# Kernel optimization log

Hardware: AMD Instinct MI355X
Metric: run time of the kernel (lower is better)

Reference implementation:

```python
import jax, jax.numpy as jnp
import numpy as np

B, N, D = 8, 4096, 256


def setup_inputs() -> dict:
    key = jax.random.key(0)
    ks = jax.random.split(key, 4)
    seq = jax.random.normal(ks[0], (B, N, D), dtype=jnp.float32)
    W_fts = jax.random.normal(ks[1], (D, D), dtype=jnp.float32) * (1.0 / np.sqrt(D))
    w_f1 = jax.random.normal(ks[2], (D, 1), dtype=jnp.float32) * (1.0 / np.sqrt(D))
    b_f1 = jnp.zeros((1,), dtype=jnp.float32)
    w_f2 = jax.random.normal(ks[3], (D, 1), dtype=jnp.float32) * (1.0 / np.sqrt(D))
    b_f2 = jnp.zeros((1,), dtype=jnp.float32)
    bias = jnp.zeros((1,), dtype=jnp.float32)
    return {"seq": seq, "W_fts": W_fts, "w_f1": w_f1, "b_f1": b_f1,
            "w_f2": w_f2, "b_f2": b_f2, "bias": bias}


def reference(seq, W_fts, w_f1, b_f1, w_f2, b_f2, bias):
    # seq: [B, N, D]
    seq_fts = jnp.einsum('bnd,de->bne', seq, W_fts)          # values, [B, N, D]
    f_1 = seq @ w_f1 + b_f1                                   # [B, N, 1]
    f_2 = seq @ w_f2 + b_f2                                   # [B, N, 1]
    logits = f_1 + jnp.swapaxes(f_2, 1, 2)                    # broadcast add -> [B, N, N]
    coefs = jax.nn.softmax(jax.nn.leaky_relu(logits, negative_slope=0.01), axis=-1)
    vals = jnp.einsum('bnm,bmd->bnd', coefs, seq_fts)         # [B, N, D]
    ret = vals + bias
    return jax.nn.relu(ret)
```

## Files before the change

kernel.cpp:

```cpp
#include <hip/hip_runtime.h>
#include <hip/hip_bf16.h>
#include <math.h>

#define B 8
#define N 4096
#define D 256
#define BN (B*N)
#define NSUP 64
#define NS1 65
#define NR1 4097

typedef __attribute__((ext_vector_type(8))) short bf16x8;
typedef __attribute__((ext_vector_type(4))) float f32x4;

#define GLD16(src, dst) __builtin_amdgcn_global_load_lds( \
    (const __attribute__((address_space(1))) void*)(src), \
    (__attribute__((address_space(3))) void*)(dst), 16, 0, 0)

__device__ __forceinline__ ushort bf16_hi(float x) {
  __hip_bfloat16 h = __float2bfloat16(x);
  return *(ushort*)&h;
}
__device__ __forceinline__ ushort bf16_lo(float x) {
  __hip_bfloat16 h = __float2bfloat16(x);
  float hf = __bfloat162float(h);
  __hip_bfloat16 l = __float2bfloat16(x - hf);
  return *(ushort*)&l;
}

__global__ __launch_bounds__(256) void k_f1f2w(const float* __restrict__ seq,
    const float* __restrict__ w1, const float* __restrict__ b1,
    const float* __restrict__ w2, const float* __restrict__ b2,
    const float* __restrict__ W, float* __restrict__ f1, float* __restrict__ f2,
    int* __restrict__ rank, ushort* __restrict__ W3) {
  if (blockIdx.x >= BN/4) {
    int n = blockIdx.x - BN/4;
    int k = threadIdx.x;
    float x = W[(size_t)k * D + n];
    ushort hu = bf16_hi(x), lu = bf16_lo(x);
    W3[(size_t)n * 768 + k] = hu;
    W3[(size_t)n * 768 + 256 + k] = lu;
    W3[(size_t)n * 768 + 512 + k] = hu;
    return;
  }
  int wave = threadIdx.x >> 6;
  int lane = threadIdx.x & 63;
  long row = (long)blockIdx.x * 4 + wave;
  float4 v = ((const float4*)(seq + row * D))[lane];
  float4 a = ((const float4*)w1)[lane];
  float4 b = ((const float4*)w2)[lane];
  float s1 = v.x*a.x + v.y*a.y + v.z*a.z + v.w*a.w;
  float s2 = v.x*b.x + v.y*b.y + v.z*b.z + v.w*b.w;
  for (int off = 32; off; off >>= 1) {
    s1 += __shfl_xor(s1, off, 64);
    s2 += __shfl_xor(s2, off, 64);
  }
  if (lane == 0) {
    f1[row] = s1 + b1[0];
    f2[row] = s2 + b2[0];
    rank[row] = 0;
  }
}

__global__ __launch_bounds__(256) void k_rank_count(const float* __restrict__ f2,
    int* __restrict__ rank) {
  __shared__ unsigned long long skey[256];
  int b = blockIdx.z;
  int tid = threadIdx.x;
  const float* fb = f2 + (long)b * N;
  int p = blockIdx.y * 256 + tid;
  unsigned int up = __float_as_uint(fb[p]);
  up ^= (unsigned int)(((int)up >> 31) | 0x80000000);
  skey[tid] = ((unsigned long long)up << 12) | (unsigned)p;
  unsigned long long kj[4];
  int jbase = blockIdx.x * 1024;
  #pragma unroll
  for (int q = 0; q < 4; ++q) {
    int j = jbase + q * 256 + tid;
    unsigned int uj = __float_as_uint(fb[j]);
    uj ^= (unsigned int)(((int)uj >> 31) | 0x80000000);
    kj[q] = ((unsigned long long)uj << 12) | (unsigned)j;
  }
  __syncthreads();
  int c[4] = {0, 0, 0, 0};
  const ulonglong2* sk2 = (const ulonglong2*)skey;
  #pragma unroll 4
  for (int pp = 0; pp < 128; ++pp) {
    ulonglong2 kk = sk2[pp];
    #pragma unroll
    for (int q = 0; q < 4; ++q) {
      c[q] += (kk.x < kj[q]) ? 1 : 0;
      c[q] += (kk.y < kj[q]) ? 1 : 0;
    }
  }
  #pragma unroll
  for (int q = 0; q < 4; ++q)
    atomicAdd(&rank[(long)b * N + jbase + q * 256 + tid], c[q]);
}

__global__ __launch_bounds__(256) void k_scatter(const float* __restrict__ f2,
    const int* __restrict__ rank, float* __restrict__ sF2, int* __restrict__ sIdx,
    float* __restrict__ e2lo, float* __restrict__ e2hi) {
  long idx = (long)blockIdx.x * 256 + threadIdx.x;
  int b = (int)(idx >> 12);
  int j = (int)(idx & (N - 1));
  float v = f2[idx];
  int cnt = rank[idx];
  long o = (long)b * N + cnt;
  sF2[o] = v;
  sIdx[o] = j;
  e2lo[o] = expf(0.01f * v);
  e2hi[o] = expf(v);
}

__global__ __launch_bounds__(256) void k_mfma(const float* __restrict__ seq,
    const int* __restrict__ sIdx, const ushort* __restrict__ W3,
    const float* __restrict__ e2lo, const float* __restrict__ e2hi,
    float* __restrict__ RelLo, float* __restrict__ RelHi,
    float* __restrict__ ZrelLo, float* __restrict__ ZrelHi,
    float* __restrict__ SupBaseLo, float* __restrict__ SupBaseHi,
    float* __restrict__ SupZlo, float* __restrict__ SupZhi) {
  __shared__ __align__(16) char smem[64 * 256 * 4];
  ushort (*As)[72] = (ushort(*)[72])smem;
  ushort (*Bs)[64] = (ushort(*)[64])(smem + 64 * 72 * 2);
  int tid = threadIdx.x;
  int wid = tid >> 6, lane = tid & 63;
  int mBase = blockIdx.x * 64;
  int b = mBase >> 12;
  int ar = tid >> 2, aq = tid & 3;
  const float* aSrc = seq + (((size_t)(b << 12)) + sIdx[mBase + ar]) * D + aq * 16;
  int lr = lane >> 3;
  int lcSw = (((lane & 7) ^ (lr & 7))) * 8;
  int wr = wid >> 1, wc = wid & 1, g = lane >> 4, r16 = lane & 15;
  int bswz = r16 & 7;

  f32x4 acc[2][8];
  #pragma unroll
  for (int m = 0; m < 2; ++m)
    #pragma unroll
    for (int n = 0; n < 8; ++n) {
      acc[m][n][0] = 0.f; acc[m][n][1] = 0.f; acc[m][n][2] = 0.f; acc[m][n][3] = 0.f;
    }

  for (int kt = 0; kt < 768; kt += 64) {
    int acol = kt & 255;
    float4 xv[4];
    #pragma unroll
    for (int i = 0; i < 4; ++i) xv[i] = *(const float4*)(aSrc + acol + i * 4);
    ushort ou[16];
    if (kt < 512) {
      #pragma unroll
      for (int i = 0; i < 4; ++i) {
        ou[i*4+0] = bf16_hi(xv[i].x); ou[i*4+1] = bf16_hi(xv[i].y);
        ou[i*4+2] = bf16_hi(xv[i].z); ou[i*4+3] = bf16_hi(xv[i].w);
      }
    } else {
      #pragma unroll
      for (int i = 0; i < 4; ++i) {
        ou[i*4+0] = bf16_lo(xv[i].x); ou[i*4+1] = bf16_lo(xv[i].y);
        ou[i*4+2] = bf16_lo(xv[i].z); ou[i*4+3] = bf16_lo(xv[i].w);
      }
    }
    __syncthreads();
    #pragma unroll
    for (int i = 0; i < 4; ++i)
      *(ushort4*)&As[ar][aq * 16 + i * 4] =
          make_ushort4(ou[i*4+0], ou[i*4+1], ou[i*4+2], ou[i*4+3]);
    #pragma unroll
    for (int q = 0; q < 8; ++q) {
      int r0 = q * 32 + wid * 8;
      GLD16(W3 + (size_t)(r0 + lr) * 768 + kt + lcSw, &Bs[r0][0]);
    }
    __syncthreads();
    #pragma unroll
    for (int kk = 0; kk < 64; kk += 32) {
      bf16x8 av[2], bv[8];
      #pragma unroll
      for (int m = 0; m < 2; ++m)
        av[m] = *(const bf16x8*)&As[wr*32 + m*16 + r16][kk + g*8];
      int jb = (kk >> 3) + g;
      int jj = jb ^ bswz;
      #pragma unroll
      for (int n = 0; n < 8; ++n) {
        int row = wc*128 + n*16 + r16;
        bv[n] = *(const bf16x8*)((const char*)Bs + row * 128 + jj * 16);
      }
      #pragma unroll
      for (int m = 0; m < 2; ++m)
        #pragma unroll
        for (int n = 0; n < 8; ++n)
          acc[m][n] = __builtin_amdgcn_mfma_f32_16x16x32_bf16(av[m], bv[n], acc[m][n], 0, 0, 0);
    }
  }

  __syncthreads();
  float (*Vt)[256] = (float(*)[256])smem;
  int cswz = (g & 3) << 2;
  #pragma unroll
  for (int m = 0; m < 2; ++m)
    #pragma unroll
    for (int n = 0; n < 8; ++n) {
      int col = (wc*128 + n*16 + r16) ^ cswz;
      #pragma unroll
      for (int j = 0; j < 4; ++j)
        Vt[wr*32 + m*16 + g*4 + j][col] = acc[m][n][j];
    }
  __syncthreads();
  int d = tid;
  int s = (mBase >> 6) & 63;
  size_t rb = (size_t)mBase;
  float rl = 0.f, rh = 0.f;
  float* pLo = RelLo + ((size_t)b * NR1 + (size_t)s * 64) * D + d;
  float* pHi = RelHi + ((size_t)b * NR1 + (size_t)s * 64) * D + d;
  #pragma unroll 8
  for (int r = 0; r < 64; ++r) {
    float wlo = e2lo[rb + r], whi = e2hi[rb + r];
    float v = Vt[r][d ^ (((r >> 2) & 3) << 2)];
    pLo[(size_t)r * D] = rl;
    pHi[(size_t)r * D] = rh;
    rl += wlo * v; rh += whi * v;
  }
  SupBaseLo[((size_t)b * NS1 + s) * D + d] = rl;
  SupBaseHi[((size_t)b * NS1 + s) * D + d] = rh;
  if (tid == 0) {
    float z = 0.f;
    #pragma unroll 8
    for (int r = 0; r < 64; ++r) { ZrelLo[(size_t)b * NR1 + s*64 + r] = z; z += e2lo[rb + r]; }
    SupZlo[b*NS1+s] = z;
  } else if (tid == 64) {
    float z = 0.f;
    #pragma unroll 8
    for (int r = 0; r < 64; ++r) { ZrelHi[(size_t)b * NR1 + s*64 + r] = z; z += e2hi[rb + r]; }
    SupZhi[b*NS1+s] = z;
  }
}

__global__ __launch_bounds__(256) void k_supscan(float* __restrict__ SupBaseLo,
    float* __restrict__ SupBaseHi, float* __restrict__ SupZlo,
    float* __restrict__ SupZhi, float* __restrict__ RelLo, float* __restrict__ RelHi,
    float* __restrict__ ZrelLo, float* __restrict__ ZrelHi) {
  int b = blockIdx.x, t = threadIdx.x;
  if (t < 64) {
    float4* lo = (float4*)SupBaseLo + (size_t)b * NS1 * 64 + t;
    float4* hi = (float4*)SupBaseHi + (size_t)b * NS1 * 64 + t;
    float4 rl = {0,0,0,0}, rh = {0,0,0,0};
    for (int s = 0; s < NSUP; s += 8) {
      float4 tl[8], th[8];
      #pragma unroll
      for (int u = 0; u < 8; ++u) { tl[u] = lo[(size_t)(s+u)*64]; th[u] = hi[(size_t)(s+u)*64]; }
      #pragma unroll
      for (int u = 0; u < 8; ++u) {
        lo[(size_t)(s+u)*64] = rl; hi[(size_t)(s+u)*64] = rh;
        rl.x+=tl[u].x; rl.y+=tl[u].y; rl.z+=tl[u].z; rl.w+=tl[u].w;
        rh.x+=th[u].x; rh.y+=th[u].y; rh.z+=th[u].z; rh.w+=th[u].w;
      }
    }
    lo[(size_t)NSUP*64] = rl;
    hi[(size_t)NSUP*64] = rh;
  } else if (t < 128) {
    float4 z = {0,0,0,0};
    ((float4*)RelLo)[((size_t)b * NR1 + 4096) * 64 + (t - 64)] = z;
  } else if (t < 192) {
    float4 z = {0,0,0,0};
    ((float4*)RelHi)[((size_t)b * NR1 + 4096) * 64 + (t - 128)] = z;
  } else if (t == 192) {
    float r = 0.f;
    for (int s = 0; s < NSUP; ++s) { float x = SupZlo[b*NS1+s]; SupZlo[b*NS1+s] = r; r += x; }
    SupZlo[b*NS1+NSUP] = r;
    ZrelLo[(size_t)b * NR1 + 4096] = 0.f;
  } else if (t == 193) {
    float r = 0.f;
    for (int s = 0; s < NSUP; ++s) { float x = SupZhi[b*NS1+s]; SupZhi[b*NS1+s] = r; r += x; }
    SupZhi[b*NS1+NSUP] = r;
    ZrelHi[(size_t)b * NR1 + 4096] = 0.f;
  }
}

__global__ __launch_bounds__(256) void k_combine2(const float* __restrict__ f1,
    const float* __restrict__ sF2,
    const float* __restrict__ RelLo, const float* __restrict__ RelHi,
    const float* __restrict__ SupBaseLo, const float* __restrict__ SupBaseHi,
    const float* __restrict__ SupZlo, const float* __restrict__ SupZhi,
    const float* __restrict__ ZrelLo, const float* __restrict__ ZrelHi,
    const float* __restrict__ bias, float* __restrict__ out) {
  int wid = threadIdx.x >> 6, lane = threadIdx.x & 63;
  size_t i = (size_t)blockIdx.x * 4 + wid;
  int b = (int)(i >> 12);
  float f1v = f1[i];
  const float* sb = sF2 + ((size_t)b << 12);
  float t = -f1v;
  int lo = 0, hi = N;
  while (lo < hi) { int mid = (lo + hi) >> 1; if (sb[mid] <= t) lo = mid + 1; else hi = mid; }
  int k = lo;
  int s = k >> 6;
  float a = expf(f1v), cc = expf(0.01f * f1v);
  float4 rl4  = ((const float4*)RelLo)[((size_t)b * NR1 + k) * 64 + lane];
  float4 rh4  = ((const float4*)RelHi)[((size_t)b * NR1 + k) * 64 + lane];
  float4 sblo = ((const float4*)SupBaseLo)[((size_t)b * NS1 + s) * 64 + lane];
  float4 sbhi = ((const float4*)SupBaseHi)[((size_t)b * NS1 + s) * 64 + lane];
  float4 pht  = ((const float4*)SupBaseHi)[((size_t)b * NS1 + NSUP) * 64 + lane];
  float Zlo = SupZlo[b*NS1+s] + ZrelLo[(size_t)b * NR1 + k];
  float Zhi = SupZhi[b*NS1+NSUP] - SupZhi[b*NS1+s] - ZrelHi[(size_t)b * NR1 + k];
  float Z = a * Zhi + cc * Zlo;
  float rz = 1.f / Z;
  float bs = bias[0];
  float4 o4;
  o4.x = fmaxf((a*(pht.x - sbhi.x - rh4.x) + cc*(sblo.x + rl4.x)) * rz + bs, 0.f);
  o4.y = fmaxf((a*(pht.y - sbhi.y - rh4.y) + cc*(sblo.y + rl4.y)) * rz + bs, 0.f);
  o4.z = fmaxf((a*(pht.z - sbhi.z - rh4.z) + cc*(sblo.z + rl4.z)) * rz + bs, 0.f);
  o4.w = fmaxf((a*(pht.w - sbhi.w - rh4.w) + cc*(sblo.w + rl4.w)) * rz + bs, 0.f);
  ((float4*)out)[i * 64 + lane] = o4;
}

extern "C" void kernel_launch(void* const* d_in, const int* in_sizes, int n_in,
                              void* d_out, int out_size, void* d_ws, size_t ws_size,
                              hipStream_t stream) {
  const float* seq  = (const float*)d_in[0];
  const float* Wf   = (const float*)d_in[1];
  const float* w1   = (const float*)d_in[2];
  const float* b1   = (const float*)d_in[3];
  const float* w2   = (const float*)d_in[4];
  const float* b2   = (const float*)d_in[5];
  const float* bias = (const float*)d_in[6];
  float* out = (float*)d_out;

  size_t need = (size_t)4 * (7*BN + 2*(size_t)B*NR1*D + 2*(size_t)B*NS1*D
              + 2*B*NS1 + 2*(size_t)B*NR1) + (size_t)256*768*2;
  if (ws_size < need) return;

  float* f1   = (float*)d_ws;
  float* f2   = f1 + BN;
  float* sF2  = f2 + BN;
  float* e2lo = sF2 + BN;
  float* e2hi = e2lo + BN;
  int* sIdx   = (int*)(e2hi + BN);
  int* rank   = sIdx + BN;
  float* RelLo = (float*)(rank + BN);
  float* RelHi = RelLo + (size_t)B * NR1 * D;
  float* SupBaseLo = RelHi + (size_t)B * NR1 * D;
  float* SupBaseHi = SupBaseLo + (size_t)B * NS1 * D;
  float* SupZlo = SupBaseHi + (size_t)B * NS1 * D;
  float* SupZhi = SupZlo + B * NS1;
  float* ZrelLo = SupZhi + B * NS1;
  float* ZrelHi = ZrelLo + (size_t)B * NR1;
  ushort* W3 = (ushort*)(ZrelHi + (size_t)B * NR1);

  k_f1f2w<<<dim3(BN/4 + 256), 256, 0, stream>>>(seq, w1, b1, w2, b2, Wf,
      f1, f2, rank, W3);
  k_rank_count<<<dim3(N/1024, N/256, B), 256, 0, stream>>>(f2, rank);
  k_scatter<<<dim3(BN/256), 256, 0, stream>>>(f2, rank, sF2, sIdx, e2lo, e2hi);
  k_mfma<<<dim3(BN/64), 256, 0, stream>>>(seq, sIdx, W3, e2lo, e2hi,
      RelLo, RelHi, ZrelLo, ZrelHi, SupBaseLo, SupBaseHi, SupZlo, SupZhi);
  k_supscan<<<dim3(B), 256, 0, stream>>>(SupBaseLo, SupBaseHi, SupZlo, SupZhi,
      RelLo, RelHi, ZrelLo, ZrelHi);
  k_combine2<<<dim3(BN/4), 256, 0, stream>>>(f1, sF2,
      RelLo, RelHi, SupBaseLo, SupBaseHi, SupZlo, SupZhi, ZrelLo, ZrelHi, bias, out);
}
```

Measured before the change: 91.53 us.

## Fuse scatter and superblock scan into producers via last-block atomics; interleave Rel

```diff
diff --git a/kernel.cpp b/kernel.cpp
--- a/kernel.cpp
+++ b/kernel.cpp
@@ -32,7 +32,7 @@
     const float* __restrict__ w1, const float* __restrict__ b1,
     const float* __restrict__ w2, const float* __restrict__ b2,
     const float* __restrict__ W, float* __restrict__ f1, float* __restrict__ f2,
-    int* __restrict__ rank, ushort* __restrict__ W3) {
+    int* __restrict__ rank, int* __restrict__ done, ushort* __restrict__ W3) {
   if (blockIdx.x >= BN/4) {
     int n = blockIdx.x - BN/4;
     int k = threadIdx.x;
@@ -43,6 +43,7 @@
     W3[(size_t)n * 768 + 512 + k] = hu;
     return;
   }
+  if (blockIdx.x == 0 && threadIdx.x < 64) done[threadIdx.x] = 0;
   int wave = threadIdx.x >> 6;
   int lane = threadIdx.x & 63;
   long row = (long)blockIdx.x * 4 + wave;
@@ -63,8 +64,10 @@
 }
 
 __global__ __launch_bounds__(256) void k_rank_count(const float* __restrict__ f2,
-    int* __restrict__ rank) {
+    int* __restrict__ rank, int* __restrict__ doneRank, float* __restrict__ sF2,
+    int* __restrict__ sIdx, float* __restrict__ e2lo, float* __restrict__ e2hi) {
   __shared__ unsigned long long skey[256];
+  __shared__ int lastFlag;
   int b = blockIdx.z;
   int tid = threadIdx.x;
   const float* fb = f2 + (long)b * N;
@@ -96,31 +99,37 @@
   #pragma unroll
   for (int q = 0; q < 4; ++q)
     atomicAdd(&rank[(long)b * N + jbase + q * 256 + tid], c[q]);
-}
-
-__global__ __launch_bounds__(256) void k_scatter(const float* __restrict__ f2,
-    const int* __restrict__ rank, float* __restrict__ sF2, int* __restrict__ sIdx,
-    float* __restrict__ e2lo, float* __restrict__ e2hi) {
-  long idx = (long)blockIdx.x * 256 + threadIdx.x;
-  int b = (int)(idx >> 12);
-  int j = (int)(idx & (N - 1));
-  float v = f2[idx];
-  int cnt = rank[idx];
-  long o = (long)b * N + cnt;
-  sF2[o] = v;
-  sIdx[o] = j;
-  e2lo[o] = expf(0.01f * v);
-  e2hi[o] = expf(v);
+  __threadfence();
+  if (tid == 0) {
+    int old = atomicAdd(&doneRank[b * 4 + blockIdx.x], 1);
+    lastFlag = (old == 15);
+  }
+  __syncthreads();
+  if (lastFlag) {
+    #pragma unroll
+    for (int q = 0; q < 4; ++q) {
+      int j = jbase + q * 256 + tid;
+      long idx = (long)b * N + j;
+      int cnt = atomicAdd(&rank[idx], 0);
+      float v = fb[j];
+      long o = (long)b * N + cnt;
+      sF2[o] = v;
+      sIdx[o] = j;
+      e2lo[o] = expf(0.01f * v);
+      e2hi[o] = expf(v);
+    }
+  }
 }
 
 __global__ __launch_bounds__(256) void k_mfma(const float* __restrict__ seq,
     const int* __restrict__ sIdx, const ushort* __restrict__ W3,
     const float* __restrict__ e2lo, const float* __restrict__ e2hi,
-    float* __restrict__ RelLo, float* __restrict__ RelHi,
-    float* __restrict__ ZrelLo, float* __restrict__ ZrelHi,
+    float* __restrict__ Rel, float* __restrict__ Zrel,
     float* __restrict__ SupBaseLo, float* __restrict__ SupBaseHi,
-    float* __restrict__ SupZlo, float* __restrict__ SupZhi) {
+    float* __restrict__ SupZlo, float* __restrict__ SupZhi,
+    int* __restrict__ doneB) {
   __shared__ __align__(16) char smem[64 * 256 * 4];
+  __shared__ int lastS;
   ushort (*As)[72] = (ushort(*)[72])smem;
   ushort (*Bs)[64] = (ushort(*)[64])(smem + 64 * 72 * 2);
   int tid = threadIdx.x;
@@ -142,11 +151,11 @@
       acc[m][n][0] = 0.f; acc[m][n][1] = 0.f; acc[m][n][2] = 0.f; acc[m][n][3] = 0.f;
     }
 
+  float4 xv[4];
+  #pragma unroll
+  for (int i = 0; i < 4; ++i) xv[i] = *(const float4*)(aSrc + i * 4);
+
   for (int kt = 0; kt < 768; kt += 64) {
-    int acol = kt & 255;
-    float4 xv[4];
-    #pragma unroll
-    for (int i = 0; i < 4; ++i) xv[i] = *(const float4*)(aSrc + acol + i * 4);
     ushort ou[16];
     if (kt < 512) {
       #pragma unroll
@@ -171,6 +180,11 @@
       int r0 = q * 32 + wid * 8;
       GLD16(W3 + (size_t)(r0 + lr) * 768 + kt + lcSw, &Bs[r0][0]);
     }
+    if (kt < 704) {
+      int nacol = (kt + 64) & 255;
+      #pragma unroll
+      for (int i = 0; i < 4; ++i) xv[i] = *(const float4*)(aSrc + nacol + i * 4);
+    }
     __syncthreads();
     #pragma unroll
     for (int kk = 0; kk < 64; kk += 32) {
@@ -210,14 +224,13 @@
   int s = (mBase >> 6) & 63;
   size_t rb = (size_t)mBase;
   float rl = 0.f, rh = 0.f;
-  float* pLo = RelLo + ((size_t)b * NR1 + (size_t)s * 64) * D + d;
-  float* pHi = RelHi + ((size_t)b * NR1 + (size_t)s * 64) * D + d;
+  float* pR = Rel + ((size_t)b * NR1 + (size_t)s * 64) * 512 + d;
   #pragma unroll 8
   for (int r = 0; r < 64; ++r) {
     float wlo = e2lo[rb + r], whi = e2hi[rb + r];
     float v = Vt[r][d ^ (((r >> 2) & 3) << 2)];
-    pLo[(size_t)r * D] = rl;
-    pHi[(size_t)r * D] = rh;
+    pR[(size_t)r * 512] = rl;
+    pR[(size_t)r * 512 + 256] = rh;
     rl += wlo * v; rh += whi * v;
   }
   SupBaseLo[((size_t)b * NS1 + s) * D + d] = rl;
@@ -225,63 +238,59 @@
   if (tid == 0) {
     float z = 0.f;
     #pragma unroll 8
-    for (int r = 0; r < 64; ++r) { ZrelLo[(size_t)b * NR1 + s*64 + r] = z; z += e2lo[rb + r]; }
+    for (int r = 0; r < 64; ++r) { Zrel[((size_t)b * NR1 + s*64 + r) * 2] = z; z += e2lo[rb + r]; }
     SupZlo[b*NS1+s] = z;
   } else if (tid == 64) {
     float z = 0.f;
     #pragma unroll 8
-    for (int r = 0; r < 64; ++r) { ZrelHi[(size_t)b * NR1 + s*64 + r] = z; z += e2hi[rb + r]; }
+    for (int r = 0; r < 64; ++r) { Zrel[((size_t)b * NR1 + s*64 + r) * 2 + 1] = z; z += e2hi[rb + r]; }
     SupZhi[b*NS1+s] = z;
   }
-}
-
-__global__ __launch_bounds__(256) void k_supscan(float* __restrict__ SupBaseLo,
-    float* __restrict__ SupBaseHi, float* __restrict__ SupZlo,
-    float* __restrict__ SupZhi, float* __restrict__ RelLo, float* __restrict__ RelHi,
-    float* __restrict__ ZrelLo, float* __restrict__ ZrelHi) {
-  int b = blockIdx.x, t = threadIdx.x;
+
+  __threadfence();
+  if (tid == 0) lastS = (atomicAdd(&doneB[b], 1) == 63);
+  __syncthreads();
+  if (!lastS) return;
+  __threadfence();
+  int t = tid;
   if (t < 64) {
     float4* lo = (float4*)SupBaseLo + (size_t)b * NS1 * 64 + t;
     float4* hi = (float4*)SupBaseHi + (size_t)b * NS1 * 64 + t;
-    float4 rl = {0,0,0,0}, rh = {0,0,0,0};
-    for (int s = 0; s < NSUP; s += 8) {
+    float4 rl4 = {0,0,0,0}, rh4 = {0,0,0,0};
+    for (int ss = 0; ss < NSUP; ss += 8) {
       float4 tl[8], th[8];
       #pragma unroll
-      for (int u = 0; u < 8; ++u) { tl[u] = lo[(size_t)(s+u)*64]; th[u] = hi[(size_t)(s+u)*64]; }
+      for (int u = 0; u < 8; ++u) { tl[u] = lo[(size_t)(ss+u)*64]; th[u] = hi[(size_t)(ss+u)*64]; }
       #pragma unroll
       for (int u = 0; u < 8; ++u) {
-        lo[(size_t)(s+u)*64] = rl; hi[(size_t)(s+u)*64] = rh;
-        rl.x+=tl[u].x; rl.y+=tl[u].y; rl.z+=tl[u].z; rl.w+=tl[u].w;
-        rh.x+=th[u].x; rh.y+=th[u].y; rh.z+=th[u].z; rh.w+=th[u].w;
+        lo[(size_t)(ss+u)*64] = rl4; hi[(size_t)(ss+u)*64] = rh4;
+        rl4.x+=tl[u].x; rl4.y+=tl[u].y; rl4.z+=tl[u].z; rl4.w+=tl[u].w;
+        rh4.x+=th[u].x; rh4.y+=th[u].y; rh4.z+=th[u].z; rh4.w+=th[u].w;
       }
     }
-    lo[(size_t)NSUP*64] = rl;
-    hi[(size_t)NSUP*64] = rh;
-  } else if (t < 128) {
-    float4 z = {0,0,0,0};
-    ((float4*)RelLo)[((size_t)b * NR1 + 4096) * 64 + (t - 64)] = z;
+    lo[(size_t)NSUP*64] = rl4;
+    hi[(size_t)NSUP*64] = rh4;
   } else if (t < 192) {
     float4 z = {0,0,0,0};
-    ((float4*)RelHi)[((size_t)b * NR1 + 4096) * 64 + (t - 128)] = z;
+    ((float4*)(Rel + ((size_t)b * NR1 + 4096) * 512))[t - 64] = z;
   } else if (t == 192) {
     float r = 0.f;
-    for (int s = 0; s < NSUP; ++s) { float x = SupZlo[b*NS1+s]; SupZlo[b*NS1+s] = r; r += x; }
+    for (int ss = 0; ss < NSUP; ++ss) { float x = SupZlo[b*NS1+ss]; SupZlo[b*NS1+ss] = r; r += x; }
     SupZlo[b*NS1+NSUP] = r;
-    ZrelLo[(size_t)b * NR1 + 4096] = 0.f;
+    Zrel[((size_t)b * NR1 + 4096) * 2] = 0.f;
   } else if (t == 193) {
     float r = 0.f;
-    for (int s = 0; s < NSUP; ++s) { float x = SupZhi[b*NS1+s]; SupZhi[b*NS1+s] = r; r += x; }
+    for (int ss = 0; ss < NSUP; ++ss) { float x = SupZhi[b*NS1+ss]; SupZhi[b*NS1+ss] = r; r += x; }
     SupZhi[b*NS1+NSUP] = r;
-    ZrelHi[(size_t)b * NR1 + 4096] = 0.f;
+    Zrel[((size_t)b * NR1 + 4096) * 2 + 1] = 0.f;
   }
 }
 
 __global__ __launch_bounds__(256) void k_combine2(const float* __restrict__ f1,
-    const float* __restrict__ sF2,
-    const float* __restrict__ RelLo, const float* __restrict__ RelHi,
+    const float* __restrict__ sF2, const float* __restrict__ Rel,
     const float* __restrict__ SupBaseLo, const float* __restrict__ SupBaseHi,
     const float* __restrict__ SupZlo, const float* __restrict__ SupZhi,
-    const float* __restrict__ ZrelLo, const float* __restrict__ ZrelHi,
+    const float* __restrict__ Zrel,
     const float* __restrict__ bias, float* __restrict__ out) {
   int wid = threadIdx.x >> 6, lane = threadIdx.x & 63;
   size_t i = (size_t)blockIdx.x * 4 + wid;
@@ -294,13 +303,15 @@
   int k = lo;
   int s = k >> 6;
   float a = expf(f1v), cc = expf(0.01f * f1v);
-  float4 rl4  = ((const float4*)RelLo)[((size_t)b * NR1 + k) * 64 + lane];
-  float4 rh4  = ((const float4*)RelHi)[((size_t)b * NR1 + k) * 64 + lane];
+  const float* rrow = Rel + ((size_t)b * NR1 + k) * 512;
+  float4 rl4 = ((const float4*)rrow)[lane];
+  float4 rh4 = ((const float4*)rrow)[64 + lane];
   float4 sblo = ((const float4*)SupBaseLo)[((size_t)b * NS1 + s) * 64 + lane];
   float4 sbhi = ((const float4*)SupBaseHi)[((size_t)b * NS1 + s) * 64 + lane];
   float4 pht  = ((const float4*)SupBaseHi)[((size_t)b * NS1 + NSUP) * 64 + lane];
-  float Zlo = SupZlo[b*NS1+s] + ZrelLo[(size_t)b * NR1 + k];
-  float Zhi = SupZhi[b*NS1+NSUP] - SupZhi[b*NS1+s] - ZrelHi[(size_t)b * NR1 + k];
+  float2 z2 = *(const float2*)(Zrel + ((size_t)b * NR1 + k) * 2);
+  float Zlo = SupZlo[b*NS1+s] + z2.x;
+  float Zhi = SupZhi[b*NS1+NSUP] - SupZhi[b*NS1+s] - z2.y;
   float Z = a * Zhi + cc * Zlo;
   float rz = 1.f / Z;
   float bs = bias[0];
@@ -324,8 +335,9 @@
   const float* bias = (const float*)d_in[6];
   float* out = (float*)d_out;
 
-  size_t need = (size_t)4 * (7*BN + 2*(size_t)B*NR1*D + 2*(size_t)B*NS1*D
-              + 2*B*NS1 + 2*(size_t)B*NR1) + (size_t)256*768*2;
+  size_t needFloats = (size_t)7*BN + (size_t)B*NR1*512 + 2*(size_t)B*NS1*D
+                    + 2*(size_t)B*NS1 + 2*(size_t)B*NR1 + 64;
+  size_t need = needFloats * 4 + (size_t)256 * 768 * 2;
   if (ws_size < need) return;
 
   float* f1   = (float*)d_ws;
@@ -335,24 +347,24 @@
   float* e2hi = e2lo + BN;
   int* sIdx   = (int*)(e2hi + BN);
   int* rank   = sIdx + BN;
-  float* RelLo = (float*)(rank + BN);
-  float* RelHi = RelLo + (size_t)B * NR1 * D;
-  float* SupBaseLo = RelHi + (size_t)B * NR1 * D;
+  float* Rel  = (float*)(rank + BN);
+  float* SupBaseLo = Rel + (size_t)B * NR1 * 512;
   float* SupBaseHi = SupBaseLo + (size_t)B * NS1 * D;
   float* SupZlo = SupBaseHi + (size_t)B * NS1 * D;
   float* SupZhi = SupZlo + B * NS1;
-  float* ZrelLo = SupZhi + B * NS1;
-  float* ZrelHi = ZrelLo + (size_t)B * NR1;
-  ushort* W3 = (ushort*)(ZrelHi + (size_t)B * NR1);
+  float* Zrel   = SupZhi + B * NS1;
+  int* done     = (int*)(Zrel + 2 * (size_t)B * NR1);
+  ushort* W3 = (ushort*)(done + 64);
+
+  int* doneRank = done;
+  int* doneB    = done + 32;
 
   k_f1f2w<<<dim3(BN/4 + 256), 256, 0, stream>>>(seq, w1, b1, w2, b2, Wf,
-      f1, f2, rank, W3);
-  k_rank_count<<<dim3(N/1024, N/256, B), 256, 0, stream>>>(f2, rank);
-  k_scatter<<<dim3(BN/256), 256, 0, stream>>>(f2, rank, sF2, sIdx, e2lo, e2hi);
+      f1, f2, rank, done, W3);
+  k_rank_count<<<dim3(N/1024, N/256, B), 256, 0, stream>>>(f2, rank, doneRank,
+      sF2, sIdx, e2lo, e2hi);
   k_mfma<<<dim3(BN/64), 256, 0, stream>>>(seq, sIdx, W3, e2lo, e2hi,
-      RelLo, RelHi, ZrelLo, ZrelHi, SupBaseLo, SupBaseHi, SupZlo, SupZhi);
-  k_supscan<<<dim3(B), 256, 0, stream>>>(SupBaseLo, SupBaseHi, SupZlo, SupZhi,
-      RelLo, RelHi, ZrelLo, ZrelHi);
-  k_combine2<<<dim3(BN/4), 256, 0, stream>>>(f1, sF2,
-      RelLo, RelHi, SupBaseLo, SupBaseHi, SupZlo, SupZhi, ZrelLo, ZrelHi, bias, out);
-}
+      Rel, Zrel, SupBaseLo, SupBaseHi, SupZlo, SupZhi, doneB);
+  k_combine2<<<dim3(BN/4), 256, 0, stream>>>(f1, sF2, Rel,
+      SupBaseLo, SupBaseHi, SupZlo, SupZhi, Zrel, bias, out);
+}
```

Result: slower. 187.1 us (+104.4%).
